# Optimization experiments

Measured on AMD Instinct MI355X. Metric: run time of the kernel, lower is better.

Reference implementation:

```python
import jax, jax.numpy as jnp
import numpy as np

N_FFT = 2048
HOP = 512


def _hann(n):
    # scipy.signal.get_window('hann', n, fftbins=True)
    return (0.5 - 0.5 * np.cos(2.0 * np.pi * np.arange(n) / n)).astype(np.float32)


def setup_inputs() -> dict:
    key = jax.random.key(0)
    k1, k2 = jax.random.split(key)
    B, T, F = 8, 1000, N_FFT // 2 + 1
    real_stft = jax.random.normal(k1, (B, 1, T, F), dtype=jnp.float32)
    imag_stft = jax.random.normal(k2, (B, 1, T, F), dtype=jnp.float32)

    # Windowed IDFT matrices, exactly as ISTFT.__init__ builds conv weights.
    n = N_FFT
    x, y = np.meshgrid(np.arange(n), np.arange(n))
    ang = 2.0 * np.pi * ((x * y) % n) / n  # angle of omega**(x*y), omega = exp(2*pi*i/n)
    win = _hann(n)  # win_length == n_fft -> pad_center is a no-op
    W_real = (np.cos(ang) / n * win[:, None]).astype(np.float32)
    W_imag = (np.sin(ang) / n * win[:, None]).astype(np.float32)

    return {
        "real_stft": real_stft,
        "imag_stft": imag_stft,
        "W_real": jnp.asarray(W_real),
        "W_imag": jnp.asarray(W_imag),
        "window": jnp.asarray(win),
        "length": 511488,  # HOP * (n_frames - 1) with n_frames = 1000
    }


def reference(real_stft, imag_stft, W_real, W_imag, window, length):
    n_fft, hop = N_FFT, HOP
    B = real_stft.shape[0]

    fr = jnp.swapaxes(real_stft[:, 0], 1, 2)  # (B, n_fft//2+1, T)
    fi = jnp.swapaxes(imag_stft[:, 0], 1, 2)
    # Hermitian symmetry -> full (B, n_fft, T) spectrum
    full_r = jnp.concatenate([fr, jnp.flip(fr[:, 1:-1, :], axis=1)], axis=1)
    full_i = jnp.concatenate([fi, -jnp.flip(fi[:, 1:-1, :], axis=1)], axis=1)

    # center=True and length given (static Python int)
    padded_length = length + n_fft
    n_frames = min(fr.shape[2], -(-padded_length // hop))

    # windowed real IFFT per frame: s[b, o, t]
    s = (jnp.einsum('oi,bit->bot', W_real, full_r[:, :, :n_frames])
         - jnp.einsum('oi,bit->bot', W_imag, full_i[:, :, :n_frames]))

    L = n_fft + hop * (n_frames - 1)
    # fused overlap-add via scatter-add
    idx = (jnp.arange(n_frames)[:, None] * hop + jnp.arange(n_fft)[None, :]).reshape(-1)
    frames = jnp.swapaxes(s, 1, 2).reshape(B, -1)  # (B, n_frames*n_fft)
    y = jnp.zeros((B, L), s.dtype).at[:, idx].add(frames)

    # window sum-square normalization (librosa.filters.window_sumsquare)
    wss = jnp.zeros((L,), window.dtype).at[idx].add(jnp.tile(window ** 2, n_frames))
    tiny = jnp.finfo(window.dtype).tiny
    nz = wss > tiny
    y = jnp.where(nz[None, :], y / jnp.where(nz, wss, 1.0)[None, :], y)

    start = n_fft // 2
    return y[:, start:start + length]
```

## Files before the change

### kernel.cpp

```cpp
#include <hip/hip_runtime.h>


#define N_FFT    2048
#define HOP      512
#define T_FRAMES 1000
#define F_BINS   1025
#define OUT_LEN  511488

#define P(a) ((a) + ((a) >> 4))

__device__ __forceinline__ void cmul(float ar, float ai, float br, float bi,
                                     float& cr, float& ci) {
    cr = ar * br - ai * bi;
    ci = ar * bi + ai * br;
}

__device__ __forceinline__ unsigned short f2bf(float f) {
    union { float f; unsigned int u; } v; v.f = f;
    unsigned int u = v.u;
    u += 0x7fffu + ((u >> 16) & 1u);
    return (unsigned short)(u >> 16);
}

__device__ __forceinline__ float bf2f(unsigned short h) {
    union { unsigned int u; float f; } v;
    v.u = ((unsigned int)h) << 16;
    return v.f;
}

__global__ __launch_bounds__(256) void istft_fft_kernel(const float* __restrict__ re,
                                                        const float* __restrict__ im,
                                                        const float* __restrict__ win,
                                                        unsigned short* __restrict__ S) {
    __shared__ float2 bufA[1088];
    __shared__ float2 bufB[1088];

    const int f   = blockIdx.x;
    const int tid = threadIdx.x;
    const float* fr = re + (size_t)f * F_BINS;
    const float* fi = im + (size_t)f * F_BINS;

    const float Sc = 0.5f / 1024.f;
    #pragma unroll
    for (int k0 = 0; k0 < 1024; k0 += 256) {
        int k = k0 + tid;
        float ar = fr[k];
        float ai = (k == 0) ? 0.f : fi[k];
        int mk = 1024 - k;
        float br = fr[mk];
        float bi = (mk == 1024) ? 0.f : fi[mk];
        float dr = ar - br, di = ai + bi;
        float ang = 3.14159265358979f * (float)k / 1024.f;
        float sn, cs;
        __sincosf(ang, &sn, &cs);
        float Zr = (ar + br - (cs * di + sn * dr)) * Sc;
        float Zi = (ai - bi + (cs * dr - sn * di)) * Sc;
        unsigned r10 = __brev((unsigned)k) >> 22;
        int rk = (int)(((r10 & 0x155u) << 1) | ((r10 >> 1) & 0x155u));
        bufA[P(rk)] = make_float2(Zr, Zi);
    }
    __syncthreads();

    float2* cur = bufA;
    float2* oth = bufB;
    #pragma unroll
    for (int s = 0; s < 5; ++s) {
        const int hm = 1 << (2 * s);
        const int j    = tid & (hm - 1);
        const int base = ((tid - j) << 2) + j;
        float ang = 1.57079632679f * (float)j / (float)hm;
        float s1, c1;
        __sincosf(ang, &s1, &c1);
        float c2, s2, c3, s3;
        cmul(c1, s1, c1, s1, c2, s2);
        cmul(c2, s2, c1, s1, c3, s3);

        int i0 = P(base), i1 = P(base + hm), i2 = P(base + 2 * hm), i3 = P(base + 3 * hm);
        float2 a = cur[i0], b = cur[i1], c = cur[i2], d = cur[i3];
        float br_, bi_, cr_, ci_, dr_, di_;
        cmul(b.x, b.y, c1, s1, br_, bi_);
        cmul(c.x, c.y, c2, s2, cr_, ci_);
        cmul(d.x, d.y, c3, s3, dr_, di_);

        float t0r = a.x + cr_, t0i = a.y + ci_;
        float t1r = a.x - cr_, t1i = a.y - ci_;
        float t2r = br_ + dr_, t2i = bi_ + di_;
        float t3r = br_ - dr_, t3i = bi_ - di_;
        oth[i0] = make_float2(t0r + t2r, t0i + t2i);
        oth[i1] = make_float2(t1r - t3i, t1i + t3r);
        oth[i2] = make_float2(t0r - t2r, t0i - t2i);
        oth[i3] = make_float2(t1r + t3i, t1i - t3r);
        __syncthreads();
        float2* tmp = cur; cur = oth; oth = tmp;
    }

    unsigned int* dst = (unsigned int*)(S + (size_t)f * N_FFT);
    const float2* w2v = (const float2*)win;
    #pragma unroll
    for (int p0 = 0; p0 < 1024; p0 += 256) {
        int p = p0 + tid;
        float2 z  = cur[P(p)];
        float2 wv = w2v[p];
        unsigned int pk = (unsigned int)f2bf(z.x * wv.x)
                        | ((unsigned int)f2bf(z.y * wv.y) << 16);
        dst[p] = pk;
    }
}

__global__ __launch_bounds__(256) void norm_kernel(const unsigned short* __restrict__ S,
                                                   const float* __restrict__ win,
                                                   float* __restrict__ out) {
    int m = blockIdx.x * 256 + threadIdx.x;
    int b = blockIdx.y;
    int n = m + N_FFT / 2;
    int thi = n >> 9; if (thi > T_FRAMES - 1) thi = T_FRAMES - 1;
    int tlo = (n - (N_FFT - HOP)) >> 9; if (tlo < 0) tlo = 0;

    float sum = 0.f, wss = 0.f;
    for (int t = tlo; t <= thi; ++t) {
        int o = n - (t << 9);
        sum += bf2f(S[((size_t)(b * T_FRAMES + t)) * N_FFT + o]);
        float w = win[o];
        wss += w * w;
    }
    out[(size_t)b * OUT_LEN + m] = (wss > 1.17549435e-38f) ? sum / wss : sum;
}

extern "C" void kernel_launch(void* const* d_in, const int* in_sizes, int n_in,
                              void* d_out, int out_size, void* d_ws, size_t ws_size,
                              hipStream_t stream) {
    const float* re  = (const float*)d_in[0];
    const float* im  = (const float*)d_in[1];
    const float* win = (const float*)d_in[4];
    float* out = (float*)d_out;

    unsigned short* S = (unsigned short*)d_ws;

    istft_fft_kernel<<<8000, 256, 0, stream>>>(re, im, win, S);
    norm_kernel<<<dim3(1998, 8), 256, 0, stream>>>(S, win, out);
}
```

Measured before the change: 148.6 us.

## Run the FFT in place with wave barriers and vectorize overlap-add normalization

The FFT kernel now works in a single shared buffer, in place. The first radix-4 stage uses no twiddles. Stages 1-3 stay inside one 64-lane wave, so the code uses wave barriers there instead of block-wide __syncthreads. The final stage is fused with the windowing and the bf16 output store, which removes a shared-memory round trip. The norm kernel now has each thread produce 8 outputs with uint4 loads and float4 stores. Interior blocks replace the per-sample window-sum-square computation with the constant 1/1.5, which holds for a Hann window at 4x overlap, and the boundary blocks keep the generic path.

Result: no change. 146.1 us (-1.7%).

```diff
diff --git a/kernel.cpp b/kernel.cpp
--- a/kernel.cpp
+++ b/kernel.cpp
@@ -32,8 +32,7 @@
                                                         const float* __restrict__ im,
                                                         const float* __restrict__ win,
                                                         unsigned short* __restrict__ S) {
-    __shared__ float2 bufA[1088];
-    __shared__ float2 bufB[1088];
+    __shared__ float2 buf[1088];
 
     const int f   = blockIdx.x;
     const int tid = threadIdx.x;
@@ -57,14 +56,27 @@
         float Zi = (ai - bi + (cs * dr - sn * di)) * Sc;
         unsigned r10 = __brev((unsigned)k) >> 22;
         int rk = (int)(((r10 & 0x155u) << 1) | ((r10 >> 1) & 0x155u));
-        bufA[P(rk)] = make_float2(Zr, Zi);
+        buf[P(rk)] = make_float2(Zr, Zi);
     }
     __syncthreads();
 
-    float2* cur = bufA;
-    float2* oth = bufB;
+    {
+        int base = tid << 2;
+        int i0 = P(base), i1 = P(base + 1), i2 = P(base + 2), i3 = P(base + 3);
+        float2 a = buf[i0], b = buf[i1], c = buf[i2], d = buf[i3];
+        float t0r = a.x + c.x, t0i = a.y + c.y;
+        float t1r = a.x - c.x, t1i = a.y - c.y;
+        float t2r = b.x + d.x, t2i = b.y + d.y;
+        float t3r = b.x - d.x, t3i = b.y - d.y;
+        buf[i0] = make_float2(t0r + t2r, t0i + t2i);
+        buf[i1] = make_float2(t1r - t3i, t1i + t3r);
+        buf[i2] = make_float2(t0r - t2r, t0i - t2i);
+        buf[i3] = make_float2(t1r + t3i, t1i - t3r);
+    }
+
     #pragma unroll
-    for (int s = 0; s < 5; ++s) {
+    for (int s = 1; s < 4; ++s) {
+        __builtin_amdgcn_wave_barrier();
         const int hm = 1 << (2 * s);
         const int j    = tid & (hm - 1);
         const int base = ((tid - j) << 2) + j;
@@ -76,7 +88,7 @@
         cmul(c2, s2, c1, s1, c3, s3);
 
         int i0 = P(base), i1 = P(base + hm), i2 = P(base + 2 * hm), i3 = P(base + 3 * hm);
-        float2 a = cur[i0], b = cur[i1], c = cur[i2], d = cur[i3];
+        float2 a = buf[i0], b = buf[i1], c = buf[i2], d = buf[i3];
         float br_, bi_, cr_, ci_, dr_, di_;
         cmul(b.x, b.y, c1, s1, br_, bi_);
         cmul(c.x, c.y, c2, s2, cr_, ci_);
@@ -86,44 +98,102 @@
         float t1r = a.x - cr_, t1i = a.y - ci_;
         float t2r = br_ + dr_, t2i = bi_ + di_;
         float t3r = br_ - dr_, t3i = bi_ - di_;
-        oth[i0] = make_float2(t0r + t2r, t0i + t2i);
-        oth[i1] = make_float2(t1r - t3i, t1i + t3r);
-        oth[i2] = make_float2(t0r - t2r, t0i - t2i);
-        oth[i3] = make_float2(t1r + t3i, t1i - t3r);
-        __syncthreads();
-        float2* tmp = cur; cur = oth; oth = tmp;
-    }
-
-    unsigned int* dst = (unsigned int*)(S + (size_t)f * N_FFT);
-    const float2* w2v = (const float2*)win;
-    #pragma unroll
-    for (int p0 = 0; p0 < 1024; p0 += 256) {
-        int p = p0 + tid;
-        float2 z  = cur[P(p)];
-        float2 wv = w2v[p];
-        unsigned int pk = (unsigned int)f2bf(z.x * wv.x)
-                        | ((unsigned int)f2bf(z.y * wv.y) << 16);
-        dst[p] = pk;
+        buf[i0] = make_float2(t0r + t2r, t0i + t2i);
+        buf[i1] = make_float2(t1r - t3i, t1i + t3r);
+        buf[i2] = make_float2(t0r - t2r, t0i - t2i);
+        buf[i3] = make_float2(t1r + t3i, t1i - t3r);
+    }
+    __syncthreads();
+
+    {
+        unsigned int* dst = (unsigned int*)(S + (size_t)f * N_FFT);
+        const float2* w2v = (const float2*)win;
+
+        float ang = 1.57079632679f * (float)tid / 256.f;
+        float s1, c1;
+        __sincosf(ang, &s1, &c1);
+        float c2, s2, c3, s3;
+        cmul(c1, s1, c1, s1, c2, s2);
+        cmul(c2, s2, c1, s1, c3, s3);
+
+        int i0 = P(tid), i1 = P(tid + 256), i2 = P(tid + 512), i3 = P(tid + 768);
+        float2 a = buf[i0], b = buf[i1], c = buf[i2], d = buf[i3];
+        float br_, bi_, cr_, ci_, dr_, di_;
+        cmul(b.x, b.y, c1, s1, br_, bi_);
+        cmul(c.x, c.y, c2, s2, cr_, ci_);
+        cmul(d.x, d.y, c3, s3, dr_, di_);
+
+        float t0r = a.x + cr_, t0i = a.y + ci_;
+        float t1r = a.x - cr_, t1i = a.y - ci_;
+        float t2r = br_ + dr_, t2i = bi_ + di_;
+        float t3r = br_ - dr_, t3i = bi_ - di_;
+
+        float2 z0 = make_float2(t0r + t2r, t0i + t2i);
+        float2 z1 = make_float2(t1r - t3i, t1i + t3r);
+        float2 z2 = make_float2(t0r - t2r, t0i - t2i);
+        float2 z3 = make_float2(t1r + t3i, t1i - t3r);
+
+        float2 w0 = w2v[tid],       w1 = w2v[tid + 256];
+        float2 w2 = w2v[tid + 512], w3 = w2v[tid + 768];
+        dst[tid]       = (unsigned int)f2bf(z0.x * w0.x) | ((unsigned int)f2bf(z0.y * w0.y) << 16);
+        dst[tid + 256] = (unsigned int)f2bf(z1.x * w1.x) | ((unsigned int)f2bf(z1.y * w1.y) << 16);
+        dst[tid + 512] = (unsigned int)f2bf(z2.x * w2.x) | ((unsigned int)f2bf(z2.y * w2.y) << 16);
+        dst[tid + 768] = (unsigned int)f2bf(z3.x * w3.x) | ((unsigned int)f2bf(z3.y * w3.y) << 16);
     }
 }
 
 __global__ __launch_bounds__(256) void norm_kernel(const unsigned short* __restrict__ S,
                                                    const float* __restrict__ win,
                                                    float* __restrict__ out) {
-    int m = blockIdx.x * 256 + threadIdx.x;
-    int b = blockIdx.y;
-    int n = m + N_FFT / 2;
-    int thi = n >> 9; if (thi > T_FRAMES - 1) thi = T_FRAMES - 1;
-    int tlo = (n - (N_FFT - HOP)) >> 9; if (tlo < 0) tlo = 0;
-
-    float sum = 0.f, wss = 0.f;
-    for (int t = tlo; t <= thi; ++t) {
-        int o = n - (t << 9);
-        sum += bf2f(S[((size_t)(b * T_FRAMES + t)) * N_FFT + o]);
-        float w = win[o];
-        wss += w * w;
-    }
-    out[(size_t)b * OUT_LEN + m] = (wss > 1.17549435e-38f) ? sum / wss : sum;
+    const int b  = blockIdx.y;
+    const int m0 = (blockIdx.x * 256 + threadIdx.x) * 8;
+
+    if (blockIdx.x >= 1 && blockIdx.x <= 248) {
+        const int n0  = m0 + N_FFT / 2;
+        const int thi = n0 >> 9;
+        const int r   = n0 & 511;
+
+        float acc[8] = {0.f, 0.f, 0.f, 0.f, 0.f, 0.f, 0.f, 0.f};
+        #pragma unroll
+        for (int kk = 0; kk < 4; ++kk) {
+            const int t = thi - kk;
+            const int o = r + (kk << 9);
+            const uint4 v = *reinterpret_cast<const uint4*>(
+                S + ((size_t)(b * T_FRAMES + t)) * N_FFT + o);
+            const unsigned int u[4] = {v.x, v.y, v.z, v.w};
+            #pragma unroll
+            for (int q = 0; q < 4; ++q) {
+                union { unsigned int u32; float f; } lo, hi;
+                lo.u32 = u[q] << 16;
+                hi.u32 = u[q] & 0xffff0000u;
+                acc[2 * q]     += lo.f;
+                acc[2 * q + 1] += hi.f;
+            }
+        }
+        const float inv = 1.f / 1.5f;
+        float* o_ptr = out + (size_t)b * OUT_LEN + m0;
+        float4 v0 = make_float4(acc[0] * inv, acc[1] * inv, acc[2] * inv, acc[3] * inv);
+        float4 v1 = make_float4(acc[4] * inv, acc[5] * inv, acc[6] * inv, acc[7] * inv);
+        reinterpret_cast<float4*>(o_ptr)[0] = v0;
+        reinterpret_cast<float4*>(o_ptr)[1] = v1;
+    } else {
+        for (int e = 0; e < 8; ++e) {
+            int m = m0 + e;
+            if (m >= OUT_LEN) continue;
+            int n = m + N_FFT / 2;
+            int thi = n >> 9; if (thi > T_FRAMES - 1) thi = T_FRAMES - 1;
+            int tlo = (n - (N_FFT - HOP)) >> 9; if (tlo < 0) tlo = 0;
+
+            float sum = 0.f, wss = 0.f;
+            for (int t = tlo; t <= thi; ++t) {
+                int o = n - (t << 9);
+                sum += bf2f(S[((size_t)(b * T_FRAMES + t)) * N_FFT + o]);
+                float w = win[o];
+                wss += w * w;
+            }
+            out[(size_t)b * OUT_LEN + m] = (wss > 1.17549435e-38f) ? sum / wss : sum;
+        }
+    }
 }
 
 extern "C" void kernel_launch(void* const* d_in, const int* in_sizes, int n_in,
@@ -137,5 +207,5 @@
     unsigned short* S = (unsigned short*)d_ws;
 
     istft_fft_kernel<<<8000, 256, 0, stream>>>(re, im, win, S);
-    norm_kernel<<<dim3(1998, 8), 256, 0, stream>>>(S, win, out);
-}
+    norm_kernel<<<dim3(250, 8), 256, 0, stream>>>(S, win, out);
+}
```
